# Kernel tuning notes

Hardware: AMD Instinct MI355X
Metric: run time of the kernel (lower is better)

## Reference

```python
import jax, jax.numpy as jnp
import numpy as np

GROUP = 16  # quantization group size along in_features
EPS = 1e-5


def _qlora_linear(x, qw, sc, b, la, lb):
    # qw: [O, I] int4 codes; sc: [O, I//GROUP] fp32 group scales
    O, I = qw.shape
    w = (qw.astype(jnp.float32).reshape(O, I // GROUP, GROUP) * sc[:, :, None]).reshape(O, I)
    base = x @ w.T + b                      # [N, O]
    lora = (x @ la.T) @ lb.T                # [N, R] @ [R, O]
    return base + lora


def _layernorm(x, g, b):
    m = jnp.mean(x, axis=-1, keepdims=True)
    v = jnp.var(x, axis=-1, keepdims=True)
    return (x - m) * jax.lax.rsqrt(v + EPS) * g + b


def setup_inputs() -> dict:
    key = jax.random.key(0)
    ks = jax.random.split(key, 8)
    N, D, R, L = 16384, 1024, 32, 18  # tokens, BIGNET_DIM, lora_dim, num linears
    x = jax.random.normal(ks[0], (N, D), jnp.float32)
    qw = jax.random.randint(ks[1], (L, D, D), -8, 8, jnp.int32)  # signed 4-bit codes
    scales = jax.random.uniform(ks[2], (L, D, D // GROUP), jnp.float32, 0.005, 0.02)
    bias = 0.01 * jax.random.normal(ks[3], (L, D), jnp.float32)
    la = 0.001 * jax.random.normal(ks[4], (L, R, D), jnp.float32)
    lb = 0.01 * jax.random.normal(ks[5], (L, D, R), jnp.float32)
    ln_g = jnp.ones((5, D), jnp.float32) + 0.1 * jax.random.normal(ks[6], (5, D), jnp.float32)
    ln_b = 0.01 * jax.random.normal(ks[7], (5, D), jnp.float32)
    return {"x": x, "qw": qw, "scales": scales, "bias": bias,
            "la": la, "lb": lb, "ln_g": ln_g, "ln_b": ln_b}


def reference(x, qw, scales, bias, la, lb, ln_g, ln_b):
    h = x
    for blk in range(6):
        y = h
        for j in range(3):
            i = blk * 3 + j
            y = _qlora_linear(y, qw[i], scales[i], bias[i], la[i], lb[i])
            if j < 2:
                y = jax.nn.relu(y)
        h = y + h  # residual
        if blk < 5:
            h = _layernorm(h, ln_g[blk], ln_b[blk])
    return h
```

## Files before the change

### kernel.cpp

```cpp
#include <hip/hip_runtime.h>

#define DIM 1024
#define NTOK 16384

typedef __attribute__((ext_vector_type(8))) _Float16 f16x8;
typedef __attribute__((ext_vector_type(4))) _Float16 f16x4;
typedef __attribute__((ext_vector_type(4))) float f32x4;

__device__ __forceinline__ void gload_lds16(const void* g, void* l) {
  __builtin_amdgcn_global_load_lds(
      (const __attribute__((address_space(1))) void*)g,
      (__attribute__((address_space(3))) void*)l, 16, 0, 0);
}

__device__ __forceinline__ f16x8 ldsr(const char* smem, int byteoff) {
  return *(const f16x8*)(smem + byteoff);
}

__device__ __forceinline__ f32x4 mfma16(f16x8 a, f16x8 b, f32x4 c) {
  return __builtin_amdgcn_mfma_f32_16x16x32_f16(a, b, c, 0, 0, 0);
}

__global__ __launch_bounds__(256) void cvt_kernel(const float* __restrict__ in,
                                                  _Float16* __restrict__ out) {
  const int i = blockIdx.x * 256 + threadIdx.x;
  float4 v = reinterpret_cast<const float4*>(in)[i];
  f16x4 o;
  o[0] = (_Float16)v.x;
  o[1] = (_Float16)v.y;
  o[2] = (_Float16)v.z;
  o[3] = (_Float16)v.w;
  *reinterpret_cast<f16x4*>(&out[(size_t)i * 4]) = o;
}

__global__ __launch_bounds__(256) void build_weff(const int* __restrict__ qw,
                                                  const float* __restrict__ scales,
                                                  const float* __restrict__ la,
                                                  const float* __restrict__ lb,
                                                  _Float16* __restrict__ W) {
  __shared__ float la_s[32][256];
  const int kt = blockIdx.x, ot = blockIdx.y, l = blockIdx.z;
  const int tid = threadIdx.x;

  for (int idx = tid; idx < 32 * 64; idx += 256) {
    const int r = idx >> 6, c4 = (idx & 63) * 4;
    *(float4*)&la_s[r][c4] =
        *(const float4*)&la[((size_t)l * 32 + r) * DIM + kt * 256 + c4];
  }
  __syncthreads();

  const int kq = tid & 31;
  const int os = tid >> 5;
  const int k0 = kq * 8;
  const int kg = kt * 256 + k0;
  const size_t robase = (size_t)l * DIM + ot * 32 + os;

  float acc[4][8];
#pragma unroll
  for (int a = 0; a < 4; ++a)
#pragma unroll
    for (int b = 0; b < 8; ++b) acc[a][b] = 0.f;

#pragma unroll 4
  for (int r = 0; r < 32; ++r) {
    const float4 lo = *(const float4*)&la_s[r][k0];
    const float4 hi = *(const float4*)&la_s[r][k0 + 4];
    const float la8[8] = {lo.x, lo.y, lo.z, lo.w, hi.x, hi.y, hi.z, hi.w};
#pragma unroll
    for (int oi = 0; oi < 4; ++oi) {
      const float lbv = lb[(robase + oi * 8) * 32 + r];
#pragma unroll
      for (int k = 0; k < 8; ++k) acc[oi][k] = fmaf(lbv, la8[k], acc[oi][k]);
    }
  }

#pragma unroll
  for (int oi = 0; oi < 4; ++oi) {
    const size_t ro = robase + oi * 8;
    const int4 q0 = *(const int4*)&qw[ro * DIM + kg];
    const int4 q1 = *(const int4*)&qw[ro * DIM + kg + 4];
    const float sc = scales[ro * 64 + (kg >> 4)];
    f16x8 o8;
    o8[0] = (_Float16)(fmaf((float)q0.x, sc, acc[oi][0]));
    o8[1] = (_Float16)(fmaf((float)q0.y, sc, acc[oi][1]));
    o8[2] = (_Float16)(fmaf((float)q0.z, sc, acc[oi][2]));
    o8[3] = (_Float16)(fmaf((float)q0.w, sc, acc[oi][3]));
    o8[4] = (_Float16)(fmaf((float)q1.x, sc, acc[oi][4]));
    o8[5] = (_Float16)(fmaf((float)q1.y, sc, acc[oi][5]));
    o8[6] = (_Float16)(fmaf((float)q1.z, sc, acc[oi][6]));
    o8[7] = (_Float16)(fmaf((float)q1.w, sc, acc[oi][7]));
    *(f16x8*)&W[ro * DIM + kg] = o8;
  }
}

#define ST_NONE ((void)0)
#define VM_NONE ((void)0)
#define VM4 asm volatile("s_waitcnt vmcnt(4)" ::: "memory")
#define VM0 asm volatile("s_waitcnt vmcnt(0)" ::: "memory")

#define RDA(BUF, FM, KS) \
  ldsr(smem, (((BUF)*2 + wm) << 14) + (((FM)*16 + r16) << 7) + (cks ^ ((KS) << 6)))
#define RDB(BUF, FN, KS)                                                        \
  ldsr(smem, 65536 + (((BUF)*2 + (wn >> 1)) << 14) +                            \
                 ((((wn & 1) * 64) + (FN)*16 + r16) << 7) + (cks ^ ((KS) << 6)))

#define PH(QQ, BUFC, STAGE, VMASM)                                          \
  {                                                                         \
    if ((QQ) == 0) {                                                        \
      _Pragma("unroll") for (int fn = 0; fn < 4; ++fn) {                    \
        bf[fn][0] = RDB(BUFC, fn, 0);                                       \
        bf[fn][1] = RDB(BUFC, fn, 1);                                       \
      }                                                                     \
    }                                                                       \
    f16x8 a00 = RDA(BUFC, 2 * (QQ), 0);                                     \
    f16x8 a01 = RDA(BUFC, 2 * (QQ), 1);                                     \
    f16x8 a10 = RDA(BUFC, 2 * (QQ) + 1, 0);                                 \
    f16x8 a11 = RDA(BUFC, 2 * (QQ) + 1, 1);                                 \
    STAGE;                                                                  \
    asm volatile("" ::: "memory");                                          \
    __builtin_amdgcn_s_barrier();                                           \
    asm volatile("s_waitcnt lgkmcnt(0)" ::: "memory");                      \
    __builtin_amdgcn_s_setprio(1);                                          \
    _Pragma("unroll") for (int fn = 0; fn < 4; ++fn) {                      \
      acc[2 * (QQ)][fn] = mfma16(a00, bf[fn][0], acc[2 * (QQ)][fn]);        \
      acc[2 * (QQ)][fn] = mfma16(a01, bf[fn][1], acc[2 * (QQ)][fn]);        \
      acc[2 * (QQ) + 1][fn] = mfma16(a10, bf[fn][0], acc[2 * (QQ) + 1][fn]); \
      acc[2 * (QQ) + 1][fn] = mfma16(a11, bf[fn][1], acc[2 * (QQ) + 1][fn]); \
    }                                                                       \
    __builtin_amdgcn_s_setprio(0);                                          \
    VMASM;                                                                  \
    asm volatile("" ::: "memory");                                          \
    __builtin_amdgcn_s_barrier();                                           \
  }

template <int MODE>
__global__ __launch_bounds__(512, 2) void qgemm(const _Float16* __restrict__ X,
                                                const _Float16* __restrict__ W,
                                                const float* __restrict__ bias,
                                                const _Float16* __restrict__ RES,
                                                void* __restrict__ OUT) {
  extern __shared__ char smem[];

  const int tid = threadIdx.x;
  const int wave = tid >> 6;
  const int lane = tid & 63;
  const int wm = wave >> 2;
  const int wn = wave & 3;
  const int bn = blockIdx.x;
  const int bm = blockIdx.y;

  const int r16 = lane & 15;
  const int cks = ((lane >> 4) * 16) ^ ((lane & 7) << 4);

  const int srl = lane >> 3;
  const int scs = ((lane & 7) ^ srl) << 3;

  f32x4 acc[8][4];
#pragma unroll
  for (int i = 0; i < 8; ++i)
#pragma unroll
    for (int j = 0; j < 4; ++j)
#pragma unroll
      for (int r = 0; r < 4; ++r) acc[i][j][r] = 0.f;

  auto stageA = [&](int buf, int h, int t) {
    const _Float16* g =
        X + (size_t)(bm * 256 + h * 128 + wave * 16 + srl) * DIM + t * 64 + scs;
    char* d = smem + (((buf * 2 + h) << 14) + wave * 2048);
    gload_lds16(g, d);
    gload_lds16(g + 8 * DIM, d + 1024);
  };
  auto stageB = [&](int buf, int h, int t) {
    const _Float16* g =
        W + (size_t)(bn * 256 + h * 128 + wave * 16 + srl) * DIM + t * 64 + scs;
    char* d = smem + (65536 + ((buf * 2 + h) << 14) + wave * 2048);
    gload_lds16(g, d);
    gload_lds16(g + 8 * DIM, d + 1024);
  };

  stageA(0, 0, 0);
  stageA(0, 1, 0);
  stageB(0, 0, 0);
  stageB(0, 1, 0);
  stageB(1, 0, 1);
  stageB(1, 1, 1);
  VM4;
  __builtin_amdgcn_s_barrier();

  f16x8 bf[4][2];

  for (int i = 0; i < 7; ++i) {
    const int t0 = 2 * i, t1 = 2 * i + 1;
    PH(0, 0, stageA(1, 0, t1), VM_NONE)
    PH(1, 0, stageA(1, 1, t1), VM_NONE)
    PH(2, 0, stageB(0, 0, t0 + 2), VM_NONE)
    PH(3, 0, stageB(0, 1, t0 + 2), VM4)
    PH(0, 1, stageA(0, 0, t0 + 2), VM_NONE)
    PH(1, 1, stageA(0, 1, t0 + 2), VM_NONE)
    PH(2, 1, stageB(1, 0, t1 + 2), VM_NONE)
    PH(3, 1, stageB(1, 1, t1 + 2), VM4)
  }
  PH(0, 0, stageA(1, 0, 15), VM_NONE)
  PH(1, 0, stageA(1, 1, 15), VM_NONE)
  PH(2, 0, ST_NONE, VM_NONE)
  PH(3, 0, ST_NONE, VM0)
  PH(0, 1, ST_NONE, VM_NONE)
  PH(1, 1, ST_NONE, VM_NONE)
  PH(2, 1, ST_NONE, VM_NONE)
  PH(3, 1, ST_NONE, VM_NONE)

  const int row0 = bm * 256 + wm * 128;
  const int col0 = bn * 256 + wn * 64;
  const int rg = (lane >> 4) * 4;
  float bv[4];
#pragma unroll
  for (int fn = 0; fn < 4; ++fn) bv[fn] = bias[col0 + fn * 16 + r16];

#pragma unroll
  for (int fm = 0; fm < 8; ++fm) {
#pragma unroll
    for (int fn = 0; fn < 4; ++fn) {
      const int col = col0 + fn * 16 + r16;
#pragma unroll
      for (int r = 0; r < 4; ++r) {
        const int row = row0 + fm * 16 + rg + r;
        float v = acc[fm][fn][r] + bv[fn];
        if (MODE == 0) {
          v = fmaxf(v, 0.f);
          ((_Float16*)OUT)[(size_t)row * DIM + col] = (_Float16)v;
        } else {
          v += (float)RES[(size_t)row * DIM + col];
          if (MODE == 1)
            ((_Float16*)OUT)[(size_t)row * DIM + col] = (_Float16)v;
          else
            ((float*)OUT)[(size_t)row * DIM + col] = v;
        }
      }
    }
  }
}

__global__ __launch_bounds__(256) void ln_kernel(const _Float16* __restrict__ in,
                                                 const float* __restrict__ g,
                                                 const float* __restrict__ b,
                                                 _Float16* __restrict__ out) {
  const int row = blockIdx.x;
  const int tid = threadIdx.x;
  const _Float16* rp = in + (size_t)row * DIM;

  f16x4 raw = reinterpret_cast<const f16x4*>(rp)[tid];
  float v0 = (float)raw[0], v1 = (float)raw[1], v2 = (float)raw[2], v3 = (float)raw[3];
  float s = v0 + v1 + v2 + v3;
  float sq = v0 * v0 + v1 * v1 + v2 * v2 + v3 * v3;
#pragma unroll
  for (int off = 32; off > 0; off >>= 1) {
    s += __shfl_down(s, off);
    sq += __shfl_down(sq, off);
  }
  __shared__ float ss[4], sq4[4];
  if ((tid & 63) == 0) {
    ss[tid >> 6] = s;
    sq4[tid >> 6] = sq;
  }
  __syncthreads();
  s = ss[0] + ss[1] + ss[2] + ss[3];
  sq = sq4[0] + sq4[1] + sq4[2] + sq4[3];
  const float mean = s * (1.f / DIM);
  const float var = sq * (1.f / DIM) - mean * mean;
  const float inv = rsqrtf(var + 1e-5f);

  float4 gv = reinterpret_cast<const float4*>(g)[tid];
  float4 bv = reinterpret_cast<const float4*>(b)[tid];
  f16x4 o;
  o[0] = (_Float16)((v0 - mean) * inv * gv.x + bv.x);
  o[1] = (_Float16)((v1 - mean) * inv * gv.y + bv.y);
  o[2] = (_Float16)((v2 - mean) * inv * gv.z + bv.z);
  o[3] = (_Float16)((v3 - mean) * inv * gv.w + bv.w);
  *reinterpret_cast<f16x4*>(&out[(size_t)row * DIM + tid * 4]) = o;
}


extern "C" void kernel_launch(void* const* d_in, const int* in_sizes, int n_in,
                              void* d_out, int out_size, void* d_ws, size_t ws_size,
                              hipStream_t stream) {
  const float* x = (const float*)d_in[0];
  const int* qw = (const int*)d_in[1];
  const float* scales = (const float*)d_in[2];
  const float* bias = (const float*)d_in[3];
  const float* la = (const float*)d_in[4];
  const float* lb = (const float*)d_in[5];
  const float* ln_g = (const float*)d_in[6];
  const float* ln_b = (const float*)d_in[7];

  char* ws = (char*)d_ws;
  const size_t WEFF_BYTES = (size_t)18 * DIM * DIM * 2;
  const size_t ACT_BYTES = (size_t)NTOK * DIM * 2;
  _Float16* Weff = (_Float16*)ws;
  _Float16* bufA = (_Float16*)(ws + WEFF_BYTES);
  _Float16* bufB = (_Float16*)(ws + WEFF_BYTES + ACT_BYTES);
  _Float16* bufC = (_Float16*)(ws + WEFF_BYTES + 2 * ACT_BYTES);

  const int LDS_BYTES = 131072;
  (void)hipFuncSetAttribute((const void*)&qgemm<0>,
                            hipFuncAttributeMaxDynamicSharedMemorySize, LDS_BYTES);
  (void)hipFuncSetAttribute((const void*)&qgemm<1>,
                            hipFuncAttributeMaxDynamicSharedMemorySize, LDS_BYTES);
  (void)hipFuncSetAttribute((const void*)&qgemm<2>,
                            hipFuncAttributeMaxDynamicSharedMemorySize, LDS_BYTES);

  cvt_kernel<<<NTOK * DIM / 1024, 256, 0, stream>>>(x, bufA);
  build_weff<<<dim3(4, 32, 18), 256, 0, stream>>>(qw, scales, la, lb, Weff);

  const dim3 ggrid(DIM / 256, NTOK / 256);
  for (int blk = 0; blk < 6; ++blk) {
    const int i0 = blk * 3;
    const size_t wstep = (size_t)DIM * DIM;
    qgemm<0><<<ggrid, 512, LDS_BYTES, stream>>>(bufA, Weff + (size_t)i0 * wstep,
                                                bias + i0 * DIM, nullptr, bufB);
    qgemm<0><<<ggrid, 512, LDS_BYTES, stream>>>(bufB, Weff + (size_t)(i0 + 1) * wstep,
                                                bias + (i0 + 1) * DIM, nullptr, bufC);
    if (blk < 5) {
      qgemm<1><<<ggrid, 512, LDS_BYTES, stream>>>(bufC, Weff + (size_t)(i0 + 2) * wstep,
                                                  bias + (i0 + 2) * DIM, bufA, bufB);
      ln_kernel<<<NTOK, 256, 0, stream>>>(bufB, ln_g + blk * DIM, ln_b + blk * DIM, bufA);
    } else {
      qgemm<2><<<ggrid, 512, LDS_BYTES, stream>>>(bufC, Weff + (size_t)(i0 + 2) * wstep,
                                                  bias + (i0 + 2) * DIM, bufA, d_out);
    }
  }
}
```

Measured before the change: 808.1 us.

## Remap GEMM tiles per XCD for L2 locality and restructure weight build kernel

The GEMM grid is flattened to 256 blocks and remapped so each XCD (block id mod 8) owns 8 contiguous row tiles with all 4 column tiles. Blocks sharing X rows and weights then hit the same L2. The weight-build kernel now uses 128-wide k tiles with twice as many blocks, stages lb in shared memory, and issues qw/scale loads before the LoRA accumulation. In exchange it writes narrower 4-byte stores and depends on round-robin dispatch of blocks across XCDs.

```diff
diff --git a/kernel.cpp b/kernel.cpp
--- a/kernel.cpp
+++ b/kernel.cpp
@@ -5,6 +5,7 @@
 
 typedef __attribute__((ext_vector_type(8))) _Float16 f16x8;
 typedef __attribute__((ext_vector_type(4))) _Float16 f16x4;
+typedef __attribute__((ext_vector_type(2))) _Float16 f16x2;
 typedef __attribute__((ext_vector_type(4))) float f32x4;
 
 __device__ __forceinline__ void gload_lds16(const void* g, void* l) {
@@ -38,58 +39,74 @@
                                                   const float* __restrict__ la,
                                                   const float* __restrict__ lb,
                                                   _Float16* __restrict__ W) {
-  __shared__ float la_s[32][256];
-  const int kt = blockIdx.x, ot = blockIdx.y, l = blockIdx.z;
+  __shared__ float la_s[32][128];
+  __shared__ float lb_s[32][32];
+  const int kt = blockIdx.x;
+  const int ot = blockIdx.y;
+  const int l = blockIdx.z;
   const int tid = threadIdx.x;
 
-  for (int idx = tid; idx < 32 * 64; idx += 256) {
-    const int r = idx >> 6, c4 = (idx & 63) * 4;
+  for (int idx = tid; idx < 32 * 32; idx += 256) {
+    const int r = idx >> 5, c4 = (idx & 31) * 4;
     *(float4*)&la_s[r][c4] =
-        *(const float4*)&la[((size_t)l * 32 + r) * DIM + kt * 256 + c4];
+        *(const float4*)&la[((size_t)l * 32 + r) * DIM + kt * 128 + c4];
+  }
+  {
+    const int o = tid >> 3, r4 = (tid & 7) * 4;
+    *(float4*)&lb_s[o][r4] =
+        *(const float4*)&lb[((size_t)l * DIM + ot * 32 + o) * 32 + r4];
   }
   __syncthreads();
 
   const int kq = tid & 31;
   const int os = tid >> 5;
-  const int k0 = kq * 8;
-  const int kg = kt * 256 + k0;
+  const int kb = 2 * kq;
   const size_t robase = (size_t)l * DIM + ot * 32 + os;
 
-  float acc[4][8];
-#pragma unroll
-  for (int a = 0; a < 4; ++a)
-#pragma unroll
-    for (int b = 0; b < 8; ++b) acc[a][b] = 0.f;
-
-#pragma unroll 4
-  for (int r = 0; r < 32; ++r) {
-    const float4 lo = *(const float4*)&la_s[r][k0];
-    const float4 hi = *(const float4*)&la_s[r][k0 + 4];
-    const float la8[8] = {lo.x, lo.y, lo.z, lo.w, hi.x, hi.y, hi.z, hi.w};
-#pragma unroll
-    for (int oi = 0; oi < 4; ++oi) {
-      const float lbv = lb[(robase + oi * 8) * 32 + r];
-#pragma unroll
-      for (int k = 0; k < 8; ++k) acc[oi][k] = fmaf(lbv, la8[k], acc[oi][k]);
-    }
-  }
-
+  int2 q[4][2];
+  float sc[4][2];
 #pragma unroll
   for (int oi = 0; oi < 4; ++oi) {
     const size_t ro = robase + oi * 8;
-    const int4 q0 = *(const int4*)&qw[ro * DIM + kg];
-    const int4 q1 = *(const int4*)&qw[ro * DIM + kg + 4];
-    const float sc = scales[ro * 64 + (kg >> 4)];
-    f16x8 o8;
-    o8[0] = (_Float16)(fmaf((float)q0.x, sc, acc[oi][0]));
-    o8[1] = (_Float16)(fmaf((float)q0.y, sc, acc[oi][1]));
-    o8[2] = (_Float16)(fmaf((float)q0.z, sc, acc[oi][2]));
-    o8[3] = (_Float16)(fmaf((float)q0.w, sc, acc[oi][3]));
-    o8[4] = (_Float16)(fmaf((float)q1.x, sc, acc[oi][4]));
-    o8[5] = (_Float16)(fmaf((float)q1.y, sc, acc[oi][5]));
-    o8[6] = (_Float16)(fmaf((float)q1.z, sc, acc[oi][6]));
-    o8[7] = (_Float16)(fmaf((float)q1.w, sc, acc[oi][7]));
-    *(f16x8*)&W[ro * DIM + kg] = o8;
+#pragma unroll
+    for (int j = 0; j < 2; ++j) {
+      const int kg = kt * 128 + kb + 64 * j;
+      q[oi][j] = *(const int2*)&qw[ro * DIM + kg];
+      sc[oi][j] = scales[ro * 64 + (kg >> 4)];
+    }
+  }
+
+  float acc[4][2][2];
+#pragma unroll
+  for (int a = 0; a < 4; ++a)
+#pragma unroll
+    for (int b = 0; b < 2; ++b) acc[a][b][0] = acc[a][b][1] = 0.f;
+
+#pragma unroll 8
+  for (int r = 0; r < 32; ++r) {
+    const float2 a0 = *(const float2*)&la_s[r][kb];
+    const float2 a1 = *(const float2*)&la_s[r][kb + 64];
+#pragma unroll
+    for (int oi = 0; oi < 4; ++oi) {
+      const float lbv = lb_s[os + 8 * oi][r];
+      acc[oi][0][0] = fmaf(lbv, a0.x, acc[oi][0][0]);
+      acc[oi][0][1] = fmaf(lbv, a0.y, acc[oi][0][1]);
+      acc[oi][1][0] = fmaf(lbv, a1.x, acc[oi][1][0]);
+      acc[oi][1][1] = fmaf(lbv, a1.y, acc[oi][1][1]);
+    }
+  }
+
+#pragma unroll
+  for (int oi = 0; oi < 4; ++oi) {
+    const size_t ro = robase + oi * 8;
+#pragma unroll
+    for (int j = 0; j < 2; ++j) {
+      const int kg = kt * 128 + kb + 64 * j;
+      f16x2 o2;
+      o2[0] = (_Float16)(fmaf((float)q[oi][j].x, sc[oi][j], acc[oi][j][0]));
+      o2[1] = (_Float16)(fmaf((float)q[oi][j].y, sc[oi][j], acc[oi][j][1]));
+      *(f16x2*)&W[ro * DIM + kg] = o2;
+    }
   }
 }
 
@@ -146,8 +163,12 @@
   const int lane = tid & 63;
   const int wm = wave >> 2;
   const int wn = wave & 3;
-  const int bn = blockIdx.x;
-  const int bm = blockIdx.y;
+
+  const int id = blockIdx.x;
+  const int xcd = id & 7;
+  const int slot = id >> 3;
+  const int bn = slot & 3;
+  const int bm = xcd * 8 + (slot >> 2);
 
   const int r16 = lane & 15;
   const int cks = ((lane >> 4) * 16) ^ ((lane & 7) << 4);
@@ -309,9 +330,9 @@
                             hipFuncAttributeMaxDynamicSharedMemorySize, LDS_BYTES);
 
   cvt_kernel<<<NTOK * DIM / 1024, 256, 0, stream>>>(x, bufA);
-  build_weff<<<dim3(4, 32, 18), 256, 0, stream>>>(qw, scales, la, lb, Weff);
-
-  const dim3 ggrid(DIM / 256, NTOK / 256);
+  build_weff<<<dim3(8, 32, 18), 256, 0, stream>>>(qw, scales, la, lb, Weff);
+
+  const dim3 ggrid(256);
   for (int blk = 0; blk < 6; ++blk) {
     const int i0 = blk * 3;
     const size_t wstep = (size_t)DIM * DIM;
```

Result: no change. 824.1 us (+2.0%).

## Swap MFMA operands for row-contiguous vector epilogue stores; restage weight-build kernel

Applied to the files above, without the earlier changes.

The GEMM swaps the A and B operands of the MFMA, so each lane's four accumulator values lie along the output column dimension instead of rows. The epilogue can then use 4-wide vector loads for bias and residual and 4-wide vector stores for the output, replacing scattered scalar fp16 stores. Separately, the effective-weight build kernel stages lb in shared memory, loads the int4 codes and scales up front, and is remapped to 4 k-columns by 8 output rows per thread. The goal is fewer, wider memory transactions in the epilogue and in weight construction. The cost is that correctness now depends on the transposed accumulator layout matching the new indexing.

```diff
diff --git a/kernel.cpp b/kernel.cpp
--- a/kernel.cpp
+++ b/kernel.cpp
@@ -39,57 +39,76 @@
                                                   const float* __restrict__ lb,
                                                   _Float16* __restrict__ W) {
   __shared__ float la_s[32][256];
-  const int kt = blockIdx.x, ot = blockIdx.y, l = blockIdx.z;
+  __shared__ float lb_s[32][32];
+  const int kt = blockIdx.x;
+  const int ot = blockIdx.y;
+  const int l = blockIdx.z;
   const int tid = threadIdx.x;
 
-  for (int idx = tid; idx < 32 * 64; idx += 256) {
+  for (int idx = tid; idx < 2048; idx += 256) {
     const int r = idx >> 6, c4 = (idx & 63) * 4;
     *(float4*)&la_s[r][c4] =
         *(const float4*)&la[((size_t)l * 32 + r) * DIM + kt * 256 + c4];
   }
+  {
+    const int o = tid >> 3, r4 = (tid & 7) * 4;
+    *(float4*)&lb_s[o][r4] =
+        *(const float4*)&lb[((size_t)l * DIM + ot * 32 + o) * 32 + r4];
+  }
   __syncthreads();
 
-  const int kq = tid & 31;
-  const int os = tid >> 5;
-  const int k0 = kq * 8;
+  const int kq = tid & 63;
+  const int os = tid >> 6;
+  const int k0 = kq * 4;
   const int kg = kt * 256 + k0;
-  const size_t robase = (size_t)l * DIM + ot * 32 + os;
-
-  float acc[4][8];
-#pragma unroll
-  for (int a = 0; a < 4; ++a)
-#pragma unroll
-    for (int b = 0; b < 8; ++b) acc[a][b] = 0.f;
-
-#pragma unroll 4
-  for (int r = 0; r < 32; ++r) {
-    const float4 lo = *(const float4*)&la_s[r][k0];
-    const float4 hi = *(const float4*)&la_s[r][k0 + 4];
-    const float la8[8] = {lo.x, lo.y, lo.z, lo.w, hi.x, hi.y, hi.z, hi.w};
-#pragma unroll
-    for (int oi = 0; oi < 4; ++oi) {
-      const float lbv = lb[(robase + oi * 8) * 32 + r];
-#pragma unroll
-      for (int k = 0; k < 8; ++k) acc[oi][k] = fmaf(lbv, la8[k], acc[oi][k]);
+  const size_t rb = (size_t)l * DIM + ot * 32 + os * 8;
+
+  int4 q[8];
+  float sc[8];
+#pragma unroll
+  for (int oi = 0; oi < 8; ++oi) {
+    q[oi] = *(const int4*)&qw[(rb + oi) * DIM + kg];
+    sc[oi] = scales[(rb + oi) * 64 + (kg >> 4)];
+  }
+
+  float acc[8][4];
+#pragma unroll
+  for (int a = 0; a < 8; ++a)
+#pragma unroll
+    for (int b = 0; b < 4; ++b) acc[a][b] = 0.f;
+
+#pragma unroll
+  for (int r4 = 0; r4 < 8; ++r4) {
+    float lbr[8][4];
+#pragma unroll
+    for (int oi = 0; oi < 8; ++oi) {
+      const float4 v = *(const float4*)&lb_s[os * 8 + oi][r4 * 4];
+      lbr[oi][0] = v.x;
+      lbr[oi][1] = v.y;
+      lbr[oi][2] = v.z;
+      lbr[oi][3] = v.w;
     }
-  }
-
-#pragma unroll
-  for (int oi = 0; oi < 4; ++oi) {
-    const size_t ro = robase + oi * 8;
-    const int4 q0 = *(const int4*)&qw[ro * DIM + kg];
-    const int4 q1 = *(const int4*)&qw[ro * DIM + kg + 4];
-    const float sc = scales[ro * 64 + (kg >> 4)];
-    f16x8 o8;
-    o8[0] = (_Float16)(fmaf((float)q0.x, sc, acc[oi][0]));
-    o8[1] = (_Float16)(fmaf((float)q0.y, sc, acc[oi][1]));
-    o8[2] = (_Float16)(fmaf((float)q0.z, sc, acc[oi][2]));
-    o8[3] = (_Float16)(fmaf((float)q0.w, sc, acc[oi][3]));
-    o8[4] = (_Float16)(fmaf((float)q1.x, sc, acc[oi][4]));
-    o8[5] = (_Float16)(fmaf((float)q1.y, sc, acc[oi][5]));
-    o8[6] = (_Float16)(fmaf((float)q1.z, sc, acc[oi][6]));
-    o8[7] = (_Float16)(fmaf((float)q1.w, sc, acc[oi][7]));
-    *(f16x8*)&W[ro * DIM + kg] = o8;
+#pragma unroll
+    for (int rr = 0; rr < 4; ++rr) {
+      const float4 a4 = *(const float4*)&la_s[r4 * 4 + rr][k0];
+#pragma unroll
+      for (int oi = 0; oi < 8; ++oi) {
+        acc[oi][0] = fmaf(lbr[oi][rr], a4.x, acc[oi][0]);
+        acc[oi][1] = fmaf(lbr[oi][rr], a4.y, acc[oi][1]);
+        acc[oi][2] = fmaf(lbr[oi][rr], a4.z, acc[oi][2]);
+        acc[oi][3] = fmaf(lbr[oi][rr], a4.w, acc[oi][3]);
+      }
+    }
+  }
+
+#pragma unroll
+  for (int oi = 0; oi < 8; ++oi) {
+    f16x4 o4;
+    o4[0] = (_Float16)(fmaf((float)q[oi].x, sc[oi], acc[oi][0]));
+    o4[1] = (_Float16)(fmaf((float)q[oi].y, sc[oi], acc[oi][1]));
+    o4[2] = (_Float16)(fmaf((float)q[oi].z, sc[oi], acc[oi][2]));
+    o4[3] = (_Float16)(fmaf((float)q[oi].w, sc[oi], acc[oi][3]));
+    *(f16x4*)&W[(rb + oi) * DIM + kg] = o4;
   }
 }
 
@@ -122,10 +141,10 @@
     asm volatile("s_waitcnt lgkmcnt(0)" ::: "memory");                      \
     __builtin_amdgcn_s_setprio(1);                                          \
     _Pragma("unroll") for (int fn = 0; fn < 4; ++fn) {                      \
-      acc[2 * (QQ)][fn] = mfma16(a00, bf[fn][0], acc[2 * (QQ)][fn]);        \
-      acc[2 * (QQ)][fn] = mfma16(a01, bf[fn][1], acc[2 * (QQ)][fn]);        \
-      acc[2 * (QQ) + 1][fn] = mfma16(a10, bf[fn][0], acc[2 * (QQ) + 1][fn]); \
-      acc[2 * (QQ) + 1][fn] = mfma16(a11, bf[fn][1], acc[2 * (QQ) + 1][fn]); \
+      acc[2 * (QQ)][fn] = mfma16(bf[fn][0], a00, acc[2 * (QQ)][fn]);        \
+      acc[2 * (QQ)][fn] = mfma16(bf[fn][1], a01, acc[2 * (QQ)][fn]);        \
+      acc[2 * (QQ) + 1][fn] = mfma16(bf[fn][0], a10, acc[2 * (QQ) + 1][fn]); \
+      acc[2 * (QQ) + 1][fn] = mfma16(bf[fn][1], a11, acc[2 * (QQ) + 1][fn]); \
     }                                                                       \
     __builtin_amdgcn_s_setprio(0);                                          \
     VMASM;                                                                  \
@@ -209,31 +228,46 @@
   PH(2, 1, ST_NONE, VM_NONE)
   PH(3, 1, ST_NONE, VM_NONE)
 
-  const int row0 = bm * 256 + wm * 128;
-  const int col0 = bn * 256 + wn * 64;
-  const int rg = (lane >> 4) * 4;
-  float bv[4];
-#pragma unroll
-  for (int fn = 0; fn < 4; ++fn) bv[fn] = bias[col0 + fn * 16 + r16];
+  const int m_base = bm * 256 + wm * 128 + r16;
+  const int o_base = bn * 256 + wn * 64 + (lane >> 4) * 4;
+  float4 bv4[4];
+#pragma unroll
+  for (int fn = 0; fn < 4; ++fn)
+    bv4[fn] = *(const float4*)&bias[o_base + fn * 16];
 
 #pragma unroll
   for (int fm = 0; fm < 8; ++fm) {
+    const size_t rowoff = (size_t)(m_base + fm * 16) * DIM;
 #pragma unroll
     for (int fn = 0; fn < 4; ++fn) {
-      const int col = col0 + fn * 16 + r16;
-#pragma unroll
-      for (int r = 0; r < 4; ++r) {
-        const int row = row0 + fm * 16 + rg + r;
-        float v = acc[fm][fn][r] + bv[fn];
-        if (MODE == 0) {
-          v = fmaxf(v, 0.f);
-          ((_Float16*)OUT)[(size_t)row * DIM + col] = (_Float16)v;
+      const int o = o_base + fn * 16;
+      float v0 = acc[fm][fn][0] + bv4[fn].x;
+      float v1 = acc[fm][fn][1] + bv4[fn].y;
+      float v2 = acc[fm][fn][2] + bv4[fn].z;
+      float v3 = acc[fm][fn][3] + bv4[fn].w;
+      if (MODE == 0) {
+        f16x4 s;
+        s[0] = (_Float16)fmaxf(v0, 0.f);
+        s[1] = (_Float16)fmaxf(v1, 0.f);
+        s[2] = (_Float16)fmaxf(v2, 0.f);
+        s[3] = (_Float16)fmaxf(v3, 0.f);
+        *(f16x4*)&((_Float16*)OUT)[rowoff + o] = s;
+      } else {
+        const f16x4 rv = *(const f16x4*)&RES[rowoff + o];
+        v0 += (float)rv[0];
+        v1 += (float)rv[1];
+        v2 += (float)rv[2];
+        v3 += (float)rv[3];
+        if (MODE == 1) {
+          f16x4 s;
+          s[0] = (_Float16)v0;
+          s[1] = (_Float16)v1;
+          s[2] = (_Float16)v2;
+          s[3] = (_Float16)v3;
+          *(f16x4*)&((_Float16*)OUT)[rowoff + o] = s;
         } else {
-          v += (float)RES[(size_t)row * DIM + col];
-          if (MODE == 1)
-            ((_Float16*)OUT)[(size_t)row * DIM + col] = (_Float16)v;
-          else
-            ((float*)OUT)[(size_t)row * DIM + col] = v;
+          float4 s = {v0, v1, v2, v3};
+          *(float4*)&((float*)OUT)[rowoff + o] = s;
         }
       }
     }
```

New measurement: 869.8 us. 7.6% more time.

## Compute LoRA weight merge with MFMA in build_weff and tweak LDS wait

Applied to the files above, without the earlier changes.

Rewrites the effective-weight builder so the lb@la rank-32 product is computed with fp16 MFMA instructions on 256x256 tiles, staging la (transposed) and lb in LDS as fp16, instead of scalar fp32 FMAs. It also adds an early partial lgkmcnt wait in the GEMM phase macro before the barrier. The LoRA delta is now computed at fp16 input precision, which adds small rounding error, and the weight-build kernel is a small share of total time.

```diff
diff --git a/kernel.cpp b/kernel.cpp
--- a/kernel.cpp
+++ b/kernel.cpp
@@ -33,63 +33,92 @@
   *reinterpret_cast<f16x4*>(&out[(size_t)i * 4]) = o;
 }
 
-__global__ __launch_bounds__(256) void build_weff(const int* __restrict__ qw,
+__global__ __launch_bounds__(512) void build_weff(const int* __restrict__ qw,
                                                   const float* __restrict__ scales,
                                                   const float* __restrict__ la,
                                                   const float* __restrict__ lb,
                                                   _Float16* __restrict__ W) {
-  __shared__ float la_s[32][256];
-  const int kt = blockIdx.x, ot = blockIdx.y, l = blockIdx.z;
+  __shared__ _Float16 laT_s[256][40];
+  __shared__ _Float16 lb_s[256][40];
+  const int kt = blockIdx.x;
+  const int ot = blockIdx.y;
+  const int l = blockIdx.z;
   const int tid = threadIdx.x;
 
-  for (int idx = tid; idx < 32 * 64; idx += 256) {
-    const int r = idx >> 6, c4 = (idx & 63) * 4;
-    *(float4*)&la_s[r][c4] =
-        *(const float4*)&la[((size_t)l * 32 + r) * DIM + kt * 256 + c4];
+#pragma unroll
+  for (int j = 0; j < 4; ++j) {
+    const int idx = tid + 512 * j;
+    const int o = idx >> 3, rg = idx & 7;
+    const float4 v = *(const float4*)&lb[((size_t)l * DIM + ot * 256 + o) * 32 + rg * 4];
+    f16x4 h;
+    h[0] = (_Float16)v.x;
+    h[1] = (_Float16)v.y;
+    h[2] = (_Float16)v.z;
+    h[3] = (_Float16)v.w;
+    *(f16x4*)&lb_s[o][rg * 4] = h;
+  }
+#pragma unroll
+  for (int j = 0; j < 4; ++j) {
+    const int idx = tid + 512 * j;
+    const int r = idx >> 6, kg = (idx & 63) * 4;
+    const float4 v = *(const float4*)&la[((size_t)l * 32 + r) * DIM + kt * 256 + kg];
+    laT_s[kg + 0][r] = (_Float16)v.x;
+    laT_s[kg + 1][r] = (_Float16)v.y;
+    laT_s[kg + 2][r] = (_Float16)v.z;
+    laT_s[kg + 3][r] = (_Float16)v.w;
   }
   __syncthreads();
 
-  const int kq = tid & 31;
-  const int os = tid >> 5;
-  const int k0 = kq * 8;
-  const int kg = kt * 256 + k0;
-  const size_t robase = (size_t)l * DIM + ot * 32 + os;
-
-  float acc[4][8];
-#pragma unroll
-  for (int a = 0; a < 4; ++a)
-#pragma unroll
-    for (int b = 0; b < 8; ++b) acc[a][b] = 0.f;
-
-#pragma unroll 4
-  for (int r = 0; r < 32; ++r) {
-    const float4 lo = *(const float4*)&la_s[r][k0];
-    const float4 hi = *(const float4*)&la_s[r][k0 + 4];
-    const float la8[8] = {lo.x, lo.y, lo.z, lo.w, hi.x, hi.y, hi.z, hi.w};
-#pragma unroll
-    for (int oi = 0; oi < 4; ++oi) {
-      const float lbv = lb[(robase + oi * 8) * 32 + r];
-#pragma unroll
-      for (int k = 0; k < 8; ++k) acc[oi][k] = fmaf(lbv, la8[k], acc[oi][k]);
+  const int wave = tid >> 6, lane = tid & 63;
+  const int wk = wave >> 1;
+  const int wkh = wave >> 2;
+  const int wo = wave & 3;
+  const int r16 = lane & 15, koff = lane >> 4;
+  (void)wk;
+
+  f32x4 acc[8][4];
+#pragma unroll
+  for (int i = 0; i < 8; ++i)
+#pragma unroll
+    for (int j = 0; j < 4; ++j)
+#pragma unroll
+      for (int r = 0; r < 4; ++r) acc[i][j][r] = 0.f;
+
+  f16x8 af[8], bfr[4];
+#pragma unroll
+  for (int fm = 0; fm < 8; ++fm)
+    af[fm] = *(const f16x8*)&laT_s[wkh * 128 + fm * 16 + r16][koff * 8];
+#pragma unroll
+  for (int fn = 0; fn < 4; ++fn)
+    bfr[fn] = *(const f16x8*)&lb_s[wo * 64 + fn * 16 + r16][koff * 8];
+
+#pragma unroll
+  for (int fm = 0; fm < 8; ++fm)
+#pragma unroll
+    for (int fn = 0; fn < 4; ++fn)
+      acc[fm][fn] = mfma16(af[fm], bfr[fn], acc[fm][fn]);
+
+  const int kg0 = kt * 256 + wkh * 128 + koff * 4;
+  const int og0 = ot * 256 + wo * 64 + r16;
+#pragma unroll
+  for (int fn = 0; fn < 4; ++fn) {
+    const size_t orow = (size_t)l * DIM + og0 + fn * 16;
+    const float4 s0 = *(const float4*)&scales[orow * 64 + kt * 16 + wkh * 8];
+    const float4 s1 = *(const float4*)&scales[orow * 64 + kt * 16 + wkh * 8 + 4];
+    const float scv[8] = {s0.x, s0.y, s0.z, s0.w, s1.x, s1.y, s1.z, s1.w};
+    int4 q[8];
+#pragma unroll
+    for (int fm = 0; fm < 8; ++fm)
+      q[fm] = *(const int4*)&qw[orow * DIM + kg0 + fm * 16];
+#pragma unroll
+    for (int fm = 0; fm < 8; ++fm) {
+      f16x4 o4;
+      o4[0] = (_Float16)fmaf((float)q[fm].x, scv[fm], acc[fm][fn][0]);
+      o4[1] = (_Float16)fmaf((float)q[fm].y, scv[fm], acc[fm][fn][1]);
+      o4[2] = (_Float16)fmaf((float)q[fm].z, scv[fm], acc[fm][fn][2]);
+      o4[3] = (_Float16)fmaf((float)q[fm].w, scv[fm], acc[fm][fn][3]);
+      *(f16x4*)&W[orow * DIM + kg0 + fm * 16] = o4;
     }
-  }
-
-#pragma unroll
-  for (int oi = 0; oi < 4; ++oi) {
-    const size_t ro = robase + oi * 8;
-    const int4 q0 = *(const int4*)&qw[ro * DIM + kg];
-    const int4 q1 = *(const int4*)&qw[ro * DIM + kg + 4];
-    const float sc = scales[ro * 64 + (kg >> 4)];
-    f16x8 o8;
-    o8[0] = (_Float16)(fmaf((float)q0.x, sc, acc[oi][0]));
-    o8[1] = (_Float16)(fmaf((float)q0.y, sc, acc[oi][1]));
-    o8[2] = (_Float16)(fmaf((float)q0.z, sc, acc[oi][2]));
-    o8[3] = (_Float16)(fmaf((float)q0.w, sc, acc[oi][3]));
-    o8[4] = (_Float16)(fmaf((float)q1.x, sc, acc[oi][4]));
-    o8[5] = (_Float16)(fmaf((float)q1.y, sc, acc[oi][5]));
-    o8[6] = (_Float16)(fmaf((float)q1.z, sc, acc[oi][6]));
-    o8[7] = (_Float16)(fmaf((float)q1.w, sc, acc[oi][7]));
-    *(f16x8*)&W[ro * DIM + kg] = o8;
   }
 }
 
@@ -117,6 +146,7 @@
     f16x8 a10 = RDA(BUFC, 2 * (QQ) + 1, 0);                                 \
     f16x8 a11 = RDA(BUFC, 2 * (QQ) + 1, 1);                                 \
     STAGE;                                                                  \
+    if ((QQ) == 0) asm volatile("s_waitcnt lgkmcnt(8)" ::: "memory");       \
     asm volatile("" ::: "memory");                                          \
     __builtin_amdgcn_s_barrier();                                           \
     asm volatile("s_waitcnt lgkmcnt(0)" ::: "memory");                      \
@@ -309,7 +339,7 @@
                             hipFuncAttributeMaxDynamicSharedMemorySize, LDS_BYTES);
 
   cvt_kernel<<<NTOK * DIM / 1024, 256, 0, stream>>>(x, bufA);
-  build_weff<<<dim3(4, 32, 18), 256, 0, stream>>>(qw, scales, la, lb, Weff);
+  build_weff<<<dim3(4, 4, 18), 512, 0, stream>>>(qw, scales, la, lb, Weff);
 
   const dim3 ggrid(DIM / 256, NTOK / 256);
   for (int blk = 0; blk < 6; ++blk) {
```

Measured after the change: 821.0 us. Within noise of the previous version (+1.6%).
